# Optimization experiments

Measured on AMD Instinct MI355X. Metric: run time of the kernel, lower is better.

Reference implementation:

```python
import jax, jax.numpy as jnp
import numpy as np

N = 100000
E = 1600000
NFEAT = 256
NHID = 128
LATENT = 64


def setup_inputs() -> dict:
    key = jax.random.key(0)
    ks = jax.random.split(key, 12)
    x = jax.random.normal(ks[0], (N, NFEAT), dtype=jnp.float32)
    edge_index = jax.random.randint(ks[1], (2, E), 0, N, dtype=jnp.int32)
    edge_weight = jax.random.uniform(ks[2], (E,), dtype=jnp.float32)
    # GraphConvolution params: uniform(-stdv, stdv), stdv = 1/sqrt(out_features)
    s1 = 1.0 / np.sqrt(NHID)
    gc1_w = jax.random.uniform(ks[3], (NFEAT, NHID), minval=-s1, maxval=s1, dtype=jnp.float32)
    gc1_b = jax.random.uniform(ks[4], (NHID,), minval=-s1, maxval=s1, dtype=jnp.float32)
    gc2_w = jax.random.uniform(ks[5], (NHID, NHID), minval=-s1, maxval=s1, dtype=jnp.float32)
    gc2_b = jax.random.uniform(ks[6], (NHID,), minval=-s1, maxval=s1, dtype=jnp.float32)
    # nn.Linear default init: uniform(-1/sqrt(fan_in), 1/sqrt(fan_in))
    s2 = 1.0 / np.sqrt(NHID)
    mu_w = jax.random.uniform(ks[7], (NHID, LATENT), minval=-s2, maxval=s2, dtype=jnp.float32)
    mu_b = jax.random.uniform(ks[8], (LATENT,), minval=-s2, maxval=s2, dtype=jnp.float32)
    lv_w = jax.random.uniform(ks[9], (NHID, LATENT), minval=-s2, maxval=s2, dtype=jnp.float32)
    lv_b = jax.random.uniform(ks[10], (LATENT,), minval=-s2, maxval=s2, dtype=jnp.float32)
    return {"x": x, "edge_index": edge_index, "edge_weight": edge_weight,
            "gc1_w": gc1_w, "gc1_b": gc1_b, "gc2_w": gc2_w, "gc2_b": gc2_b,
            "mu_w": mu_w, "mu_b": mu_b, "lv_w": lv_w, "lv_b": lv_b}


def _spmm(edge_index, edge_weight, support):
    # out[row] += w * support[col]  (sparse adj @ dense support)
    row, col = edge_index[0], edge_index[1]
    msgs = support[col] * edge_weight[:, None]          # [E, F]
    return jax.ops.segment_sum(msgs, row, num_segments=N)


def reference(x, edge_index, edge_weight, gc1_w, gc1_b, gc2_w, gc2_b,
              mu_w, mu_b, lv_w, lv_b):
    # gc1: mm -> spmm -> bias -> relu (dropout is identity in eval mode)
    h = jax.nn.relu(_spmm(edge_index, edge_weight, x @ gc1_w) + gc1_b)
    h = jax.nn.relu(_spmm(edge_index, edge_weight, h @ gc2_w) + gc2_b)
    mu = h @ mu_w + mu_b
    log_var = h @ lv_w + lv_b
    return mu, log_var
```

## Files before the change

### kernel.cpp

```cpp
#include <hip/hip_runtime.h>
#include <hip/hip_fp16.h>

#define N_NODES 100000
#define N_EDGES 1600000
#define NFEAT   256
#define NHID    128
#define LATENT  64

#define NBUCKET 782
#define NBLKH   196
#define CHUNK   8192
#define NHIST   (NBUCKET * NBLKH)
#define NHISTT  300

#define NGEMM1B 3125
#define FR_HIST NGEMM1B
#define FR_W2   (FR_HIST + NBLKH)
#define FR_W3   (FR_W2 + 8)
#define FR_TOT  (FR_W3 + 8)

typedef __attribute__((ext_vector_type(8))) short s16x8;
typedef __attribute__((ext_vector_type(4))) float f32x4;

__device__ __forceinline__ unsigned short f2bf(float f) {
    union { float f; unsigned u; } v; v.f = f;
    unsigned r = v.u + 0x7fffu + ((v.u >> 16) & 1u);
    return (unsigned short)(r >> 16);
}
__device__ __forceinline__ float bflo(unsigned u) {
    union { unsigned x; float f; } v; v.x = u << 16; return v.f;
}
__device__ __forceinline__ float bfhi(unsigned u) {
    union { unsigned x; float f; } v; v.x = u & 0xffff0000u; return v.f;
}
__device__ __forceinline__ float w15_decode(unsigned pv) {
    return __half2float(__ushort_as_half((unsigned short)(pv & 0x7fffu)));
}

__device__ __forceinline__ int incl_scan512(int v, int t, int (&s)[2][512]) {
    s[0][t] = v;
    __syncthreads();
    int p = 0;
    for (int off = 1; off < 512; off <<= 1) {
        int x = s[p][t];
        if (t >= off) x += s[p][t - off];
        s[p ^ 1][t] = x;
        p ^= 1;
        __syncthreads();
    }
    return s[p][t];
}


__device__ __forceinline__ void prep_body(
    int c, int K, int Ntot, int ncol0, int ldb0, int ldb1,
    const float* __restrict__ B0, const float* __restrict__ B1,
    unsigned short* __restrict__ out)
{
    int K8 = K >> 3;
    int total = (Ntot >> 4) * K8 * 16;
    if (c >= total) return;
    int m  = c & 15;
    int kc = (c >> 4) % K8;
    int nt = (c >> 4) / K8;
    int col = nt * 16 + m;
    const float* src; int ld, cc;
    if (col < ncol0) { src = B0; ld = ldb0; cc = col; }
    else             { src = B1; ld = ldb1; cc = col - ncol0; }
    s16x8 v;
    #pragma unroll
    for (int j = 0; j < 8; ++j)
        v[j] = (short)f2bf(src[(size_t)(kc * 8 + j) * ld + cc]);
    *(s16x8*)&out[(size_t)c * 8] = v;
}


template<int AMODE, int BMODE, int OMODE>
__device__ __forceinline__ void gemm_body(
    int bm, int t, int K,
    const float* __restrict__ A32, const unsigned short* __restrict__ A16,
    const unsigned short* __restrict__ Bpre, const float* __restrict__ Bf32,
    unsigned short* __restrict__ C16,
    float* __restrict__ C0, float* __restrict__ C1,
    const float* __restrict__ bias0, const float* __restrict__ bias1)
{
    __shared__ unsigned short As[2048];
    __shared__ unsigned short Bs[8192];

    const int m0   = bm * 32;
    const int lane = t & 63;
    const int w    = t >> 6;
    const int rt   = w & 1;
    const int ntb  = (w >> 1) * 4;
    const int fm   = lane & 15;
    const int q    = lane >> 4;
    const int K8   = K >> 3;

    f32x4 acc[4] = {};

    for (int kt = 0; kt < K; kt += 64) {
        {
            int r = t >> 3, kc = t & 7;
            int lo = ((r >> 4) * 8 + kc) * 128 + (r & 15) * 8;
            if (AMODE == 0) {
                const float* g = A32 + (size_t)(m0 + r) * K + kt + kc * 8;
                float4 a = *(const float4*)g;
                float4 b = *(const float4*)(g + 4);
                s16x8 v;
                v[0] = (short)f2bf(a.x); v[1] = (short)f2bf(a.y);
                v[2] = (short)f2bf(a.z); v[3] = (short)f2bf(a.w);
                v[4] = (short)f2bf(b.x); v[5] = (short)f2bf(b.y);
                v[6] = (short)f2bf(b.z); v[7] = (short)f2bf(b.w);
                *(s16x8*)&As[lo] = v;
            } else {
                const unsigned short* g = A16 + (size_t)(m0 + r) * 128 + kt + kc * 8;
                *(s16x8*)&As[lo] = *(const s16x8*)g;
            }
        }
        {
            int ktc = kt >> 3;
            #pragma unroll
            for (int i = 0; i < 4; ++i) {
                int c  = t + i * 256;
                int nt = c >> 7, kc = (c >> 4) & 7, m = c & 15;
                if (BMODE == 1) {
                    const unsigned short* g =
                        Bpre + ((size_t)(nt * K8 + ktc + kc) * 16 + m) * 8;
                    *(s16x8*)&Bs[c * 8] = *(const s16x8*)g;
                } else {
                    int col = nt * 16 + m;
                    const float* g = Bf32 + (size_t)(kt + kc * 8) * 128 + col;
                    s16x8 v;
                    #pragma unroll
                    for (int j = 0; j < 8; ++j)
                        v[j] = (short)f2bf(g[(size_t)j * 128]);
                    *(s16x8*)&Bs[c * 8] = v;
                }
            }
        }
        __syncthreads();
        #pragma unroll
        for (int kk = 0; kk < 2; ++kk) {
            int kcq = kk * 4 + q;
            s16x8 a = *(const s16x8*)&As[(rt * 8 + kcq) * 128 + fm * 8];
            #pragma unroll
            for (int i = 0; i < 4; ++i) {
                s16x8 b = *(const s16x8*)&Bs[((ntb + i) * 8 + kcq) * 128 + fm * 8];
                acc[i] = __builtin_amdgcn_mfma_f32_16x16x32_bf16(a, b, acc[i], 0, 0, 0);
            }
        }
        __syncthreads();
    }

    #pragma unroll
    for (int i = 0; i < 4; ++i) {
        int col = (ntb + i) * 16 + fm;
        #pragma unroll
        for (int j = 0; j < 4; ++j) {
            int r = m0 + rt * 16 + q * 4 + j;
            float v = acc[i][j];
            if (OMODE == 0) {
                C16[(size_t)r * 128 + col] = f2bf(v);
            } else {
                if (col < 64) C0[(size_t)r * 64 + col]      = v + bias0[col];
                else          C1[(size_t)r * 64 + col - 64] = v + bias1[col - 64];
            }
        }
    }
}


__global__ __launch_bounds__(256) void k_front(
    const float* __restrict__ x, const int* __restrict__ rows,
    int* __restrict__ histG,
    const float* __restrict__ gc1_w, unsigned short* __restrict__ bufSup,
    const float* __restrict__ gc2_w, unsigned short* __restrict__ w2p,
    const float* __restrict__ mu_w, const float* __restrict__ lv_w,
    unsigned short* __restrict__ w3p)
{
    int b = blockIdx.x;
    int t = threadIdx.x;
    if (b < NGEMM1B) {
        gemm_body<0, 0, 0>(b, t, NFEAT, x, nullptr, nullptr, gc1_w,
                           bufSup, nullptr, nullptr, nullptr, nullptr);
    } else if (b < FR_W2) {
        __shared__ int hist[NBUCKET];
        int hb = b - FR_HIST;
        for (int i = t; i < NBUCKET; i += 256) hist[i] = 0;
        __syncthreads();
        int base = hb * CHUNK;
        #pragma unroll 4
        for (int i = 0; i < CHUNK / 256; ++i) {
            int e = base + i * 256 + t;
            if (e < N_EDGES) {
                int r = rows[e];
                atomicAdd(&hist[r >> 7], 1);
            }
        }
        __syncthreads();
        for (int i = t; i < NBUCKET; i += 256)
            histG[(size_t)i * NBLKH + hb] = hist[i];
    } else if (b < FR_W3) {
        prep_body((b - FR_W2) * 256 + t, NHID, NHID, NHID, NHID, NHID, gc2_w, gc2_w, w2p);
    } else {
        prep_body((b - FR_W3) * 256 + t, NHID, NHID, LATENT, LATENT, LATENT, mu_w, lv_w, w3p);
    }
}


__global__ __launch_bounds__(512) void k_scanA(
    const int* __restrict__ histG, int* __restrict__ hist_excl,
    int* __restrict__ hbsum)
{
    __shared__ int s[2][512];
    int b = blockIdx.x, t = threadIdx.x;
    int i = b * 512 + t;
    int v = (i < NHIST) ? histG[i] : 0;
    int incl = incl_scan512(v, t, s);
    if (i < NHIST) hist_excl[i] = incl - v;
    if (t == 511) hbsum[b] = incl;
}


__global__ __launch_bounds__(512) void k_scatterA(
    const int* __restrict__ rows, const int* __restrict__ cols,
    const float* __restrict__ ew,
    const int* __restrict__ hist_excl, const int* __restrict__ hbsum,
    unsigned* __restrict__ tmp_pv, unsigned char* __restrict__ tmp_row,
    int* __restrict__ bucket_start)
{
    __shared__ int s[2][512];
    __shared__ int tbase[NHISTT];
    __shared__ int cur[NBUCKET];
    int b = blockIdx.x, t = threadIdx.x;
    int v = (t < NHISTT) ? hbsum[t] : 0;
    int incl = incl_scan512(v, t, s);
    if (t < NHISTT) tbase[t] = incl - v;
    __syncthreads();
    for (int i = t; i < NBUCKET; i += 512) {
        int idx = i * NBLKH + b;
        int val = hist_excl[idx] + tbase[idx >> 9];
        cur[i] = val;
        if (b == 0) bucket_start[i] = val;
    }
    __syncthreads();
    int base = b * CHUNK;
    #pragma unroll 4
    for (int i = 0; i < CHUNK / 512; ++i) {
        int e = base + i * 512 + t;
        if (e < N_EDGES) {
            int r = rows[e];
            unsigned hv = (unsigned)__half_as_ushort(__float2half(ew[e]));
            unsigned pv = ((unsigned)cols[e] << 15) | (hv & 0x7fffu);
            int p = atomicAdd(&cur[r >> 7], 1);
            tmp_pv[p]  = pv;
            tmp_row[p] = (unsigned char)(r & 127);
        }
    }
}


__global__ __launch_bounds__(256) void k_passB(
    const int* __restrict__ bucket_start, const unsigned* __restrict__ tmp_pv,
    const unsigned char* __restrict__ tmp_row,
    unsigned* __restrict__ ecw, int* __restrict__ row_ptr)
{
    __shared__ int cnt[128];
    __shared__ int sc[2][128];
    __shared__ int cur[128];
    int b  = blockIdx.x;
    int t  = threadIdx.x;
    int r0 = b * 128;
    int beg = bucket_start[b];
    int end = (b + 1 < NBUCKET) ? bucket_start[b + 1] : N_EDGES;
    if (t < 128) cnt[t] = 0;
    __syncthreads();
    for (int e = beg + t; e < end; e += 256)
        atomicAdd(&cnt[tmp_row[e]], 1);
    __syncthreads();
    int p = 0;
    if (t < 128) sc[0][t] = cnt[t];
    __syncthreads();
    for (int off = 1; off < 128; off <<= 1) {
        if (t < 128) {
            int x = sc[p][t];
            if (t >= off) x += sc[p][t - off];
            sc[p ^ 1][t] = x;
        }
        p ^= 1;
        __syncthreads();
    }
    if (t < 128) {
        int excl = sc[p][t] - cnt[t];
        int rr = r0 + t;
        if (rr < N_NODES) row_ptr[rr] = beg + excl;
        cur[t] = beg + excl;
    }
    if (b == NBUCKET - 1 && t == 0) row_ptr[N_NODES] = N_EDGES;
    __syncthreads();
    for (int e = beg + t; e < end; e += 256) {
        unsigned pv = tmp_pv[e];
        int pos = atomicAdd(&cur[tmp_row[e]], 1);
        ecw[pos] = pv;
    }
}


template<int AMODE, int OMODE>
__global__ __launch_bounds__(256) void k_gemm(
    int K, const float* __restrict__ A32, const unsigned short* __restrict__ A16,
    const unsigned short* __restrict__ Bpre,
    unsigned short* __restrict__ C16,
    float* __restrict__ C0, float* __restrict__ C1,
    const float* __restrict__ bias0, const float* __restrict__ bias1)
{
    gemm_body<AMODE, 1, OMODE>(blockIdx.x, threadIdx.x, K, A32, A16, Bpre,
                               nullptr, C16, C0, C1, bias0, bias1);
}


#define EDGE4(qq, vv, aa0, aa1, aa2, aa3)                \
    {                                                    \
        float ww = w15_decode(qq);                       \
        aa0 += ww * bflo(vv.x);                          \
        aa1 += ww * bfhi(vv.x);                          \
        aa2 += ww * bflo(vv.y);                          \
        aa3 += ww * bfhi(vv.y);                          \
    }

__global__ __launch_bounds__(256) void k_spmm(const int* __restrict__ row_ptr,
                                              const unsigned* __restrict__ ecw,
                                              const unsigned short* __restrict__ sup,
                                              const float* __restrict__ bias,
                                              unsigned short* __restrict__ out) {
    int wave = threadIdx.x >> 6;
    int lane = threadIdx.x & 63;
    int row  = blockIdx.x * 4 + wave;
    if (row >= N_NODES) return;
    int half = lane >> 5;
    int fl   = lane & 31;

    int beg = row_ptr[row];
    int end = row_ptr[row + 1];
    float a0 = 0.f, a1 = 0.f, a2 = 0.f, a3 = 0.f;
    float b0 = 0.f, b1 = 0.f, b2 = 0.f, b3 = 0.f;

    int e = beg;
    for (; e + 16 <= end; e += 16) {
        unsigned q0 = ecw[e + 0 + half];
        unsigned q1 = ecw[e + 2 + half];
        unsigned q2 = ecw[e + 4 + half];
        unsigned q3 = ecw[e + 6 + half];
        unsigned q4 = ecw[e + 8 + half];
        unsigned q5 = ecw[e + 10 + half];
        unsigned q6 = ecw[e + 12 + half];
        unsigned q7 = ecw[e + 14 + half];
        uint2 v0 = *(const uint2*)(sup + (size_t)(q0 >> 15) * NHID + fl * 4);
        uint2 v1 = *(const uint2*)(sup + (size_t)(q1 >> 15) * NHID + fl * 4);
        uint2 v2 = *(const uint2*)(sup + (size_t)(q2 >> 15) * NHID + fl * 4);
        uint2 v3 = *(const uint2*)(sup + (size_t)(q3 >> 15) * NHID + fl * 4);
        uint2 v4 = *(const uint2*)(sup + (size_t)(q4 >> 15) * NHID + fl * 4);
        uint2 v5 = *(const uint2*)(sup + (size_t)(q5 >> 15) * NHID + fl * 4);
        uint2 v6 = *(const uint2*)(sup + (size_t)(q6 >> 15) * NHID + fl * 4);
        uint2 v7 = *(const uint2*)(sup + (size_t)(q7 >> 15) * NHID + fl * 4);
        EDGE4(q0, v0, a0, a1, a2, a3)
        EDGE4(q1, v1, b0, b1, b2, b3)
        EDGE4(q2, v2, a0, a1, a2, a3)
        EDGE4(q3, v3, b0, b1, b2, b3)
        EDGE4(q4, v4, a0, a1, a2, a3)
        EDGE4(q5, v5, b0, b1, b2, b3)
        EDGE4(q6, v6, a0, a1, a2, a3)
        EDGE4(q7, v7, b0, b1, b2, b3)
    }
    for (; e + 8 <= end; e += 8) {
        unsigned q0 = ecw[e + 0 + half];
        unsigned q1 = ecw[e + 2 + half];
        unsigned q2 = ecw[e + 4 + half];
        unsigned q3 = ecw[e + 6 + half];
        uint2 v0 = *(const uint2*)(sup + (size_t)(q0 >> 15) * NHID + fl * 4);
        uint2 v1 = *(const uint2*)(sup + (size_t)(q1 >> 15) * NHID + fl * 4);
        uint2 v2 = *(const uint2*)(sup + (size_t)(q2 >> 15) * NHID + fl * 4);
        uint2 v3 = *(const uint2*)(sup + (size_t)(q3 >> 15) * NHID + fl * 4);
        EDGE4(q0, v0, a0, a1, a2, a3)
        EDGE4(q1, v1, b0, b1, b2, b3)
        EDGE4(q2, v2, a0, a1, a2, a3)
        EDGE4(q3, v3, b0, b1, b2, b3)
    }
    if (e < end) {
        int last = end - 1;
        int e0 = e + 0 + half, e1 = e + 2 + half;
        int e2 = e + 4 + half, e3 = e + 6 + half;
        unsigned q0 = ecw[e0 <= last ? e0 : last];
        unsigned q1 = ecw[e1 <= last ? e1 : last];
        unsigned q2 = ecw[e2 <= last ? e2 : last];
        unsigned q3 = ecw[e3 <= last ? e3 : last];
        uint2 v0 = *(const uint2*)(sup + (size_t)(q0 >> 15) * NHID + fl * 4);
        uint2 v1 = *(const uint2*)(sup + (size_t)(q1 >> 15) * NHID + fl * 4);
        uint2 v2 = *(const uint2*)(sup + (size_t)(q2 >> 15) * NHID + fl * 4);
        uint2 v3 = *(const uint2*)(sup + (size_t)(q3 >> 15) * NHID + fl * 4);
        float w0 = (e0 <= last) ? w15_decode(q0) : 0.f;
        float w1 = (e1 <= last) ? w15_decode(q1) : 0.f;
        float w2 = (e2 <= last) ? w15_decode(q2) : 0.f;
        float w3 = (e3 <= last) ? w15_decode(q3) : 0.f;
        a0 += w0 * bflo(v0.x); a1 += w0 * bfhi(v0.x);
        a2 += w0 * bflo(v0.y); a3 += w0 * bfhi(v0.y);
        b0 += w1 * bflo(v1.x); b1 += w1 * bfhi(v1.x);
        b2 += w1 * bflo(v1.y); b3 += w1 * bfhi(v1.y);
        a0 += w2 * bflo(v2.x); a1 += w2 * bfhi(v2.x);
        a2 += w2 * bflo(v2.y); a3 += w2 * bfhi(v2.y);
        b0 += w3 * bflo(v3.x); b1 += w3 * bfhi(v3.x);
        b2 += w3 * bflo(v3.y); b3 += w3 * bfhi(v3.y);
    }

    a0 += b0; a1 += b1; a2 += b2; a3 += b3;
    a0 += __shfl_xor(a0, 32, 64);
    a1 += __shfl_xor(a1, 32, 64);
    a2 += __shfl_xor(a2, 32, 64);
    a3 += __shfl_xor(a3, 32, 64);

    if (half == 0) {
        float o0 = a0 + bias[fl * 4 + 0];
        float o1 = a1 + bias[fl * 4 + 1];
        float o2 = a2 + bias[fl * 4 + 2];
        float o3 = a3 + bias[fl * 4 + 3];
        o0 = o0 > 0.f ? o0 : 0.f;
        o1 = o1 > 0.f ? o1 : 0.f;
        o2 = o2 > 0.f ? o2 : 0.f;
        o3 = o3 > 0.f ? o3 : 0.f;
        uint2 pv;
        pv.x = (unsigned)f2bf(o0) | ((unsigned)f2bf(o1) << 16);
        pv.y = (unsigned)f2bf(o2) | ((unsigned)f2bf(o3) << 16);
        *(uint2*)(out + (size_t)row * NHID + fl * 4) = pv;
    }
}


extern "C" void kernel_launch(void* const* d_in, const int* in_sizes, int n_in,
                              void* d_out, int out_size, void* d_ws, size_t ws_size,
                              hipStream_t stream) {
    const float* x     = (const float*)d_in[0];
    const int*   ei    = (const int*)  d_in[1];
    const float* ew    = (const float*)d_in[2];
    const float* gc1_w = (const float*)d_in[3];
    const float* gc1_b = (const float*)d_in[4];
    const float* gc2_w = (const float*)d_in[5];
    const float* gc2_b = (const float*)d_in[6];
    const float* mu_w  = (const float*)d_in[7];
    const float* mu_b  = (const float*)d_in[8];
    const float* lv_w  = (const float*)d_in[9];
    const float* lv_b  = (const float*)d_in[10];
    float* out = (float*)d_out;

    const int* rows = ei;
    const int* cols = ei + N_EDGES;

    char* p = (char*)d_ws;
    auto alloc = [&](size_t bytes) {
        char* r = p;
        p += (bytes + 255) & ~(size_t)255;
        return r;
    };
    int*      row_ptr      = (int*)     alloc((size_t)(N_NODES + 1) * 4);
    int*      histG        = (int*)     alloc((size_t)NHIST * 4);
    int*      hist_excl    = (int*)     alloc((size_t)NHIST * 4);
    int*      hbsum        = (int*)     alloc((size_t)NHISTT * 4);
    int*      bucket_start = (int*)     alloc((size_t)NBUCKET * 4);
    unsigned* ecw          = (unsigned*)alloc((size_t)N_EDGES * 4);
    unsigned* tmp_pv       = (unsigned*)alloc((size_t)N_EDGES * 4);
    unsigned char* tmp_row = (unsigned char*)alloc((size_t)N_EDGES);
    unsigned short* w2p    = (unsigned short*)alloc((size_t)NHID * NHID * 2);
    unsigned short* w3p    = (unsigned short*)alloc((size_t)NHID * NHID * 2);
    unsigned short* bufSup = (unsigned short*)alloc((size_t)N_NODES * NHID * 2);
    unsigned short* bufH   = (unsigned short*)alloc((size_t)N_NODES * NHID * 2);
    (void)ws_size; (void)n_in; (void)in_sizes; (void)out_size;

    k_front<<<FR_TOT, 256, 0, stream>>>(x, rows, histG, gc1_w, bufSup,
                                        gc2_w, w2p, mu_w, lv_w, w3p);
    k_scanA<<<NHISTT, 512, 0, stream>>>(histG, hist_excl, hbsum);
    k_scatterA<<<NBLKH, 512, 0, stream>>>(rows, cols, ew, hist_excl, hbsum,
                                          tmp_pv, tmp_row, bucket_start);
    k_passB<<<NBUCKET, 256, 0, stream>>>(bucket_start, tmp_pv, tmp_row, ecw, row_ptr);

    k_spmm<<<N_NODES / 4, 256, 0, stream>>>(row_ptr, ecw, bufSup, gc1_b, bufH);
    k_gemm<1, 0><<<N_NODES / 32, 256, 0, stream>>>(NHID, nullptr, bufH, w2p,
                                                   bufSup, nullptr, nullptr, nullptr, nullptr);
    k_spmm<<<N_NODES / 4, 256, 0, stream>>>(row_ptr, ecw, bufSup, gc2_b, bufH);
    k_gemm<1, 1><<<N_NODES / 32, 256, 0, stream>>>(NHID, nullptr, bufH, w3p,
                                                   nullptr, out, out + (size_t)N_NODES * LATENT,
                                                   mu_b, lv_b);
}
```

Baseline: 438.9 us.

## Split first GEMM out of front kernel and prepack gc1 weights to bf16

The first x@gc1_w GEMM no longer runs inside the combined front kernel alongside the histogram and weight-prep blocks. It becomes its own launch after CSR construction and reads gc1_w from a prepacked bf16 layout instead of converting strided fp32 weights per tile. This removes redundant per-block weight conversion and the mixed-role block layout. In exchange, the GEMM no longer overlaps with histogramming and adds a separate launch.

New measurement: 434.4 us. No clear change (-1.0%).

```diff
diff --git a/kernel.cpp b/kernel.cpp
--- a/kernel.cpp
+++ b/kernel.cpp
@@ -12,12 +12,6 @@
 #define CHUNK   8192
 #define NHIST   (NBUCKET * NBLKH)
 #define NHISTT  300
-
-#define NGEMM1B 3125
-#define FR_HIST NGEMM1B
-#define FR_W2   (FR_HIST + NBLKH)
-#define FR_W3   (FR_W2 + 8)
-#define FR_TOT  (FR_W3 + 8)
 
 typedef __attribute__((ext_vector_type(8))) short s16x8;
 typedef __attribute__((ext_vector_type(4))) float f32x4;
@@ -75,11 +69,143 @@
 }
 
 
-template<int AMODE, int BMODE, int OMODE>
-__device__ __forceinline__ void gemm_body(
-    int bm, int t, int K,
-    const float* __restrict__ A32, const unsigned short* __restrict__ A16,
-    const unsigned short* __restrict__ Bpre, const float* __restrict__ Bf32,
+__global__ __launch_bounds__(256) void k_pre(
+    const int* __restrict__ rows, int* __restrict__ histG,
+    const float* __restrict__ gc1_w, unsigned short* __restrict__ w1p,
+    const float* __restrict__ gc2_w, unsigned short* __restrict__ w2p,
+    const float* __restrict__ mu_w, const float* __restrict__ lv_w,
+    unsigned short* __restrict__ w3p)
+{
+    int b = blockIdx.x;
+    int t = threadIdx.x;
+    if (b < NBLKH) {
+        __shared__ int hist[NBUCKET];
+        for (int i = t; i < NBUCKET; i += 256) hist[i] = 0;
+        __syncthreads();
+        int base = b * CHUNK;
+        #pragma unroll 4
+        for (int i = 0; i < CHUNK / 256; ++i) {
+            int e = base + i * 256 + t;
+            if (e < N_EDGES) {
+                int r = rows[e];
+                atomicAdd(&hist[r >> 7], 1);
+            }
+        }
+        __syncthreads();
+        for (int i = t; i < NBUCKET; i += 256)
+            histG[(size_t)i * NBLKH + b] = hist[i];
+    } else if (b < NBLKH + 16) {
+        prep_body((b - NBLKH) * 256 + t, NFEAT, NHID, NHID, NHID, NHID, gc1_w, gc1_w, w1p);
+    } else if (b < NBLKH + 24) {
+        prep_body((b - NBLKH - 16) * 256 + t, NHID, NHID, NHID, NHID, NHID, gc2_w, gc2_w, w2p);
+    } else {
+        prep_body((b - NBLKH - 24) * 256 + t, NHID, NHID, LATENT, LATENT, LATENT, mu_w, lv_w, w3p);
+    }
+}
+
+
+__global__ __launch_bounds__(512) void k_scanA(
+    const int* __restrict__ histG, int* __restrict__ hist_excl,
+    int* __restrict__ hbsum)
+{
+    __shared__ int s[2][512];
+    int b = blockIdx.x, t = threadIdx.x;
+    int i = b * 512 + t;
+    int v = (i < NHIST) ? histG[i] : 0;
+    int incl = incl_scan512(v, t, s);
+    if (i < NHIST) hist_excl[i] = incl - v;
+    if (t == 511) hbsum[b] = incl;
+}
+
+
+__global__ __launch_bounds__(512) void k_scatterA(
+    const int* __restrict__ rows, const int* __restrict__ cols,
+    const float* __restrict__ ew,
+    const int* __restrict__ hist_excl, const int* __restrict__ hbsum,
+    unsigned* __restrict__ tmp_pv, unsigned char* __restrict__ tmp_row,
+    int* __restrict__ bucket_start)
+{
+    __shared__ int s[2][512];
+    __shared__ int tbase[NHISTT];
+    __shared__ int cur[NBUCKET];
+    int b = blockIdx.x, t = threadIdx.x;
+    int v = (t < NHISTT) ? hbsum[t] : 0;
+    int incl = incl_scan512(v, t, s);
+    if (t < NHISTT) tbase[t] = incl - v;
+    __syncthreads();
+    for (int i = t; i < NBUCKET; i += 512) {
+        int idx = i * NBLKH + b;
+        int val = hist_excl[idx] + tbase[idx >> 9];
+        cur[i] = val;
+        if (b == 0) bucket_start[i] = val;
+    }
+    __syncthreads();
+    int base = b * CHUNK;
+    #pragma unroll 4
+    for (int i = 0; i < CHUNK / 512; ++i) {
+        int e = base + i * 512 + t;
+        if (e < N_EDGES) {
+            int r = rows[e];
+            unsigned hv = (unsigned)__half_as_ushort(__float2half(ew[e]));
+            unsigned pv = ((unsigned)cols[e] << 15) | (hv & 0x7fffu);
+            int p = atomicAdd(&cur[r >> 7], 1);
+            tmp_pv[p]  = pv;
+            tmp_row[p] = (unsigned char)(r & 127);
+        }
+    }
+}
+
+
+__global__ __launch_bounds__(256) void k_passB(
+    const int* __restrict__ bucket_start, const unsigned* __restrict__ tmp_pv,
+    const unsigned char* __restrict__ tmp_row,
+    unsigned* __restrict__ ecw, int* __restrict__ row_ptr)
+{
+    __shared__ int cnt[128];
+    __shared__ int sc[2][128];
+    __shared__ int cur[128];
+    int b  = blockIdx.x;
+    int t  = threadIdx.x;
+    int r0 = b * 128;
+    int beg = bucket_start[b];
+    int end = (b + 1 < NBUCKET) ? bucket_start[b + 1] : N_EDGES;
+    if (t < 128) cnt[t] = 0;
+    __syncthreads();
+    for (int e = beg + t; e < end; e += 256)
+        atomicAdd(&cnt[tmp_row[e]], 1);
+    __syncthreads();
+    int p = 0;
+    if (t < 128) sc[0][t] = cnt[t];
+    __syncthreads();
+    for (int off = 1; off < 128; off <<= 1) {
+        if (t < 128) {
+            int x = sc[p][t];
+            if (t >= off) x += sc[p][t - off];
+            sc[p ^ 1][t] = x;
+        }
+        p ^= 1;
+        __syncthreads();
+    }
+    if (t < 128) {
+        int excl = sc[p][t] - cnt[t];
+        int rr = r0 + t;
+        if (rr < N_NODES) row_ptr[rr] = beg + excl;
+        cur[t] = beg + excl;
+    }
+    if (b == NBUCKET - 1 && t == 0) row_ptr[N_NODES] = N_EDGES;
+    __syncthreads();
+    for (int e = beg + t; e < end; e += 256) {
+        unsigned pv = tmp_pv[e];
+        int pos = atomicAdd(&cur[tmp_row[e]], 1);
+        ecw[pos] = pv;
+    }
+}
+
+
+template<int AMODE, int OMODE>
+__global__ __launch_bounds__(256) void k_gemm(
+    int K, const float* __restrict__ A32, const unsigned short* __restrict__ A16,
+    const unsigned short* __restrict__ Bpre,
     unsigned short* __restrict__ C16,
     float* __restrict__ C0, float* __restrict__ C1,
     const float* __restrict__ bias0, const float* __restrict__ bias1)
@@ -87,7 +213,8 @@
     __shared__ unsigned short As[2048];
     __shared__ unsigned short Bs[8192];
 
-    const int m0   = bm * 32;
+    const int t    = threadIdx.x;
+    const int m0   = blockIdx.x * 32;
     const int lane = t & 63;
     const int w    = t >> 6;
     const int rt   = w & 1;
@@ -123,19 +250,9 @@
             for (int i = 0; i < 4; ++i) {
                 int c  = t + i * 256;
                 int nt = c >> 7, kc = (c >> 4) & 7, m = c & 15;
-                if (BMODE == 1) {
-                    const unsigned short* g =
-                        Bpre + ((size_t)(nt * K8 + ktc + kc) * 16 + m) * 8;
-                    *(s16x8*)&Bs[c * 8] = *(const s16x8*)g;
-                } else {
-                    int col = nt * 16 + m;
-                    const float* g = Bf32 + (size_t)(kt + kc * 8) * 128 + col;
-                    s16x8 v;
-                    #pragma unroll
-                    for (int j = 0; j < 8; ++j)
-                        v[j] = (short)f2bf(g[(size_t)j * 128]);
-                    *(s16x8*)&Bs[c * 8] = v;
-                }
+                const unsigned short* g =
+                    Bpre + ((size_t)(nt * K8 + ktc + kc) * 16 + m) * 8;
+                *(s16x8*)&Bs[c * 8] = *(const s16x8*)g;
             }
         }
         __syncthreads();
@@ -167,155 +284,6 @@
             }
         }
     }
-}
-
-
-__global__ __launch_bounds__(256) void k_front(
-    const float* __restrict__ x, const int* __restrict__ rows,
-    int* __restrict__ histG,
-    const float* __restrict__ gc1_w, unsigned short* __restrict__ bufSup,
-    const float* __restrict__ gc2_w, unsigned short* __restrict__ w2p,
-    const float* __restrict__ mu_w, const float* __restrict__ lv_w,
-    unsigned short* __restrict__ w3p)
-{
-    int b = blockIdx.x;
-    int t = threadIdx.x;
-    if (b < NGEMM1B) {
-        gemm_body<0, 0, 0>(b, t, NFEAT, x, nullptr, nullptr, gc1_w,
-                           bufSup, nullptr, nullptr, nullptr, nullptr);
-    } else if (b < FR_W2) {
-        __shared__ int hist[NBUCKET];
-        int hb = b - FR_HIST;
-        for (int i = t; i < NBUCKET; i += 256) hist[i] = 0;
-        __syncthreads();
-        int base = hb * CHUNK;
-        #pragma unroll 4
-        for (int i = 0; i < CHUNK / 256; ++i) {
-            int e = base + i * 256 + t;
-            if (e < N_EDGES) {
-                int r = rows[e];
-                atomicAdd(&hist[r >> 7], 1);
-            }
-        }
-        __syncthreads();
-        for (int i = t; i < NBUCKET; i += 256)
-            histG[(size_t)i * NBLKH + hb] = hist[i];
-    } else if (b < FR_W3) {
-        prep_body((b - FR_W2) * 256 + t, NHID, NHID, NHID, NHID, NHID, gc2_w, gc2_w, w2p);
-    } else {
-        prep_body((b - FR_W3) * 256 + t, NHID, NHID, LATENT, LATENT, LATENT, mu_w, lv_w, w3p);
-    }
-}
-
-
-__global__ __launch_bounds__(512) void k_scanA(
-    const int* __restrict__ histG, int* __restrict__ hist_excl,
-    int* __restrict__ hbsum)
-{
-    __shared__ int s[2][512];
-    int b = blockIdx.x, t = threadIdx.x;
-    int i = b * 512 + t;
-    int v = (i < NHIST) ? histG[i] : 0;
-    int incl = incl_scan512(v, t, s);
-    if (i < NHIST) hist_excl[i] = incl - v;
-    if (t == 511) hbsum[b] = incl;
-}
-
-
-__global__ __launch_bounds__(512) void k_scatterA(
-    const int* __restrict__ rows, const int* __restrict__ cols,
-    const float* __restrict__ ew,
-    const int* __restrict__ hist_excl, const int* __restrict__ hbsum,
-    unsigned* __restrict__ tmp_pv, unsigned char* __restrict__ tmp_row,
-    int* __restrict__ bucket_start)
-{
-    __shared__ int s[2][512];
-    __shared__ int tbase[NHISTT];
-    __shared__ int cur[NBUCKET];
-    int b = blockIdx.x, t = threadIdx.x;
-    int v = (t < NHISTT) ? hbsum[t] : 0;
-    int incl = incl_scan512(v, t, s);
-    if (t < NHISTT) tbase[t] = incl - v;
-    __syncthreads();
-    for (int i = t; i < NBUCKET; i += 512) {
-        int idx = i * NBLKH + b;
-        int val = hist_excl[idx] + tbase[idx >> 9];
-        cur[i] = val;
-        if (b == 0) bucket_start[i] = val;
-    }
-    __syncthreads();
-    int base = b * CHUNK;
-    #pragma unroll 4
-    for (int i = 0; i < CHUNK / 512; ++i) {
-        int e = base + i * 512 + t;
-        if (e < N_EDGES) {
-            int r = rows[e];
-            unsigned hv = (unsigned)__half_as_ushort(__float2half(ew[e]));
-            unsigned pv = ((unsigned)cols[e] << 15) | (hv & 0x7fffu);
-            int p = atomicAdd(&cur[r >> 7], 1);
-            tmp_pv[p]  = pv;
-            tmp_row[p] = (unsigned char)(r & 127);
-        }
-    }
-}
-
-
-__global__ __launch_bounds__(256) void k_passB(
-    const int* __restrict__ bucket_start, const unsigned* __restrict__ tmp_pv,
-    const unsigned char* __restrict__ tmp_row,
-    unsigned* __restrict__ ecw, int* __restrict__ row_ptr)
-{
-    __shared__ int cnt[128];
-    __shared__ int sc[2][128];
-    __shared__ int cur[128];
-    int b  = blockIdx.x;
-    int t  = threadIdx.x;
-    int r0 = b * 128;
-    int beg = bucket_start[b];
-    int end = (b + 1 < NBUCKET) ? bucket_start[b + 1] : N_EDGES;
-    if (t < 128) cnt[t] = 0;
-    __syncthreads();
-    for (int e = beg + t; e < end; e += 256)
-        atomicAdd(&cnt[tmp_row[e]], 1);
-    __syncthreads();
-    int p = 0;
-    if (t < 128) sc[0][t] = cnt[t];
-    __syncthreads();
-    for (int off = 1; off < 128; off <<= 1) {
-        if (t < 128) {
-            int x = sc[p][t];
-            if (t >= off) x += sc[p][t - off];
-            sc[p ^ 1][t] = x;
-        }
-        p ^= 1;
-        __syncthreads();
-    }
-    if (t < 128) {
-        int excl = sc[p][t] - cnt[t];
-        int rr = r0 + t;
-        if (rr < N_NODES) row_ptr[rr] = beg + excl;
-        cur[t] = beg + excl;
-    }
-    if (b == NBUCKET - 1 && t == 0) row_ptr[N_NODES] = N_EDGES;
-    __syncthreads();
-    for (int e = beg + t; e < end; e += 256) {
-        unsigned pv = tmp_pv[e];
-        int pos = atomicAdd(&cur[tmp_row[e]], 1);
-        ecw[pos] = pv;
-    }
-}
-
-
-template<int AMODE, int OMODE>
-__global__ __launch_bounds__(256) void k_gemm(
-    int K, const float* __restrict__ A32, const unsigned short* __restrict__ A16,
-    const unsigned short* __restrict__ Bpre,
-    unsigned short* __restrict__ C16,
-    float* __restrict__ C0, float* __restrict__ C1,
-    const float* __restrict__ bias0, const float* __restrict__ bias1)
-{
-    gemm_body<AMODE, 1, OMODE>(blockIdx.x, threadIdx.x, K, A32, A16, Bpre,
-                               nullptr, C16, C0, C1, bias0, bias1);
 }
 
 
@@ -468,19 +436,22 @@
     unsigned* ecw          = (unsigned*)alloc((size_t)N_EDGES * 4);
     unsigned* tmp_pv       = (unsigned*)alloc((size_t)N_EDGES * 4);
     unsigned char* tmp_row = (unsigned char*)alloc((size_t)N_EDGES);
+    unsigned short* w1p    = (unsigned short*)alloc((size_t)NFEAT * NHID * 2);
     unsigned short* w2p    = (unsigned short*)alloc((size_t)NHID * NHID * 2);
     unsigned short* w3p    = (unsigned short*)alloc((size_t)NHID * NHID * 2);
     unsigned short* bufSup = (unsigned short*)alloc((size_t)N_NODES * NHID * 2);
     unsigned short* bufH   = (unsigned short*)alloc((size_t)N_NODES * NHID * 2);
     (void)ws_size; (void)n_in; (void)in_sizes; (void)out_size;
 
-    k_front<<<FR_TOT, 256, 0, stream>>>(x, rows, histG, gc1_w, bufSup,
-                                        gc2_w, w2p, mu_w, lv_w, w3p);
+    k_pre<<<NBLKH + 32, 256, 0, stream>>>(rows, histG,
+                                          gc1_w, w1p, gc2_w, w2p, mu_w, lv_w, w3p);
     k_scanA<<<NHISTT, 512, 0, stream>>>(histG, hist_excl, hbsum);
     k_scatterA<<<NBLKH, 512, 0, stream>>>(rows, cols, ew, hist_excl, hbsum,
                                           tmp_pv, tmp_row, bucket_start);
     k_passB<<<NBUCKET, 256, 0, stream>>>(bucket_start, tmp_pv, tmp_row, ecw, row_ptr);
 
+    k_gemm<0, 0><<<N_NODES / 32, 256, 0, stream>>>(NFEAT, x, nullptr, w1p,
+                                                   bufSup, nullptr, nullptr, nullptr, nullptr);
     k_spmm<<<N_NODES / 4, 256, 0, stream>>>(row_ptr, ecw, bufSup, gc1_b, bufH);
     k_gemm<1, 0><<<N_NODES / 32, 256, 0, stream>>>(NHID, nullptr, bufH, w2p,
                                                    bufSup, nullptr, nullptr, nullptr, nullptr);
```
